# Kernel tuning notes

Hardware: AMD Instinct MI355X
Metric: run time of the kernel (lower is better)

## Reference

```python
import jax, jax.numpy as jnp
import numpy as np

B, H, F, Z, T = 4096, 512, 256, 64, 16
IN = Z + H + F  # LSTM input dim

def _dense_params(key, din, dout, scale=0.05):
    kw, kb = jax.random.split(key)
    return (jax.random.normal(kw, (din, dout), jnp.float32) * scale,
            jax.random.normal(kb, (dout,), jnp.float32) * scale)

def setup_inputs() -> dict:
    key = jax.random.key(0)
    ks = jax.random.split(key, 16)
    inp = {
        'h_i': jax.random.normal(ks[0], (B, H), jnp.float32),
        'eps_inf': jax.random.normal(ks[1], (T, B, Z), jnp.float32),
        'eps_pri': jax.random.normal(ks[2], (T, B, Z), jnp.float32),
        'Wx': jax.random.normal(ks[3], (IN, 4 * H), jnp.float32) * 0.05,
        'Wh': jax.random.normal(ks[4], (H, 4 * H), jnp.float32) * 0.05,
        'b_lstm': jnp.zeros((4 * H,), jnp.float32),
    }
    dims = [(H, F), (F, F), (F, F),            # dense1-3
            (2 * H + 2 * F, Z), (Z, Z), (Z, Z),  # dense4-6 (inference)
            (2 * H + F, Z), (Z, Z), (Z, Z)]      # dense7-9 (prior)
    for i, (di, do) in enumerate(dims):
        w, b = _dense_params(ks[5 + i], di, do)
        inp[f'W{i+1}'] = w
        inp[f'b{i+1}'] = b
    return inp

def reference(h_i, eps_inf, eps_pri, Wx, Wh, b_lstm,
              W1, b1, W2, b2, W3, b3, W4, b4, W5, b5,
              W6, b6, W7, b7, W8, b8, W9, b9):
    relu = jax.nn.relu
    batch = h_i.shape[0]

    def step(carry, eps):
        h, c, z_j, y_prev = carry
        e_inf, e_pri = eps
        x_j = jnp.concatenate([z_j, h_i, y_prev], axis=1)  # [B, Z+H+F]
        gates = x_j @ Wx + h @ Wh + b_lstm                 # [B, 4H]
        i_g, f_g, g_g, o_g = jnp.split(gates, 4, axis=1)   # keras order i,f,c,o
        c_new = jax.nn.sigmoid(f_g) * c + jax.nn.sigmoid(i_g) * jnp.tanh(g_g)
        h_new = jax.nn.sigmoid(o_g) * jnp.tanh(c_new)
        # decoder MLP on LSTM output
        y_j = relu(relu(relu(h_new @ W1 + b1) @ W2 + b2) @ W3 + b3)  # [B, F]
        s_j = c_new  # state[1] is the cell state in keras LSTMCell
        # inference network
        inf_in = jnp.concatenate([h_i, s_j, y_j, y_prev], axis=1)
        h_z = relu(inf_in @ W4 + b4)
        mean_j = relu(h_z @ W5 + b5)
        log_var_j = relu(h_z @ W6 + b6)
        z_new = mean_j + e_inf * jnp.sqrt(jnp.exp(log_var_j))
        # prior network
        pri_in = jnp.concatenate([h_i, s_j, y_prev], axis=1)
        h_z_ = relu(pri_in @ W7 + b7)
        mean_j_ = relu(h_z_ @ W8 + b8)
        log_var_j_ = relu(h_z_ @ W9 + b9)
        z_prior = mean_j_ + e_pri * jnp.sqrt(jnp.exp(log_var_j_))
        return (h_new, c_new, z_new, y_j), (y_j, mean_j, log_var_j, z_new, z_prior)

    init = (jnp.zeros((batch, Wh.shape[0]), h_i.dtype),
            jnp.zeros((batch, Wh.shape[0]), h_i.dtype),
            jnp.zeros((batch, W5.shape[1]), h_i.dtype),
            jnp.zeros((batch, W1.shape[1]), h_i.dtype))
    _, (ys, means, log_vars, z_post, z_pri) = jax.lax.scan(step, init, (eps_inf, eps_pri))
    fake_input = jnp.transpose(ys, (1, 0, 2))     # [B, T, F]
    mean_all = jnp.transpose(means, (1, 0, 2))    # [B, T, Z]
    log_var_all = jnp.transpose(log_vars, (1, 0, 2))
    z_all = jnp.stack([z_post, z_pri], axis=1)    # [T, 2, B, Z]
    return fake_input, mean_all, log_var_all, z_all
```

## Files before the change

kernel.cpp:

```cpp
#include <hip/hip_runtime.h>


typedef __attribute__((ext_vector_type(8))) short short8;
typedef __attribute__((ext_vector_type(4))) float f32x4;

#define Bt 4096
#define Hd 512
#define Fd 256
#define Zd 64
#define Td 16

#define OFF_WG   0
#define OFF_WPH  212992
#define OFF_W1   344064
#define OFF_W2   360448
#define OFF_W3   368640
#define OFF_W4D  376832
#define OFF_W4H  385024
#define OFF_W7D  389120
#define OFF_W7H  395264
#define OFF_W5   399360
#define OFF_W6   399872
#define OFF_W8   400384
#define OFF_W9   400896

#define O1 16777216
#define O2 20971520
#define O3 25165824

__device__ inline short f2bf(float f) {
  unsigned u = __builtin_bit_cast(unsigned, f);
  unsigned r = (u + 0x7FFFu + ((u >> 16) & 1u)) >> 16;
  return (short)(unsigned short)r;
}
__device__ inline float sigm(float x) { return 1.f / (1.f + __expf(-x)); }
__device__ inline float tanhx(float x) { return 1.f - 2.f / (__expf(2.f * x) + 1.f); }

__global__ void conv_frag(const float* s0, int k0, const float* s1, int k1,
                          const float* s2, int k2, int N, short8* dst, int KT,
                          int total) {
  int idx = blockIdx.x * blockDim.x + threadIdx.x;
  if (idx >= total) return;
  int lane = idx & 63;
  int tt = idx >> 6;
  int kt = tt % KT;
  int nt = tt / KT;
  int c = nt * 16 + (lane & 15);
  int kb = kt * 32 + (lane >> 4) * 8;
  short8 v;
#pragma unroll
  for (int j = 0; j < 8; ++j) {
    int kc = kb + j;
    float f;
    if (kc < k0) f = s0[kc * N + c];
    else if (kc < k0 + k1) f = s1[(kc - k0) * N + c];
    else f = s2[(kc - k0 - k1) * N + c];
    v[j] = f2bf(f);
  }
  dst[idx] = v;
}

struct Params {
  const float* h_i; const float* eps_inf; const float* eps_pri;
  const float* b_lstm;
  const float *b1, *b2, *b3, *b4, *b5, *b6, *b7, *b8, *b9;
  const short8 *WG, *WPH, *W1f, *W2f, *W3f, *W4d, *W4h, *W7d, *W7h,
               *W5f, *W6f, *W8f, *W9f;
  float* out;
};

#define A1S 840
#define A4S 1032
#define TS  264
#define HZS 72

#define MFMA(a, b, c) __builtin_amdgcn_mfma_f32_16x16x32_bf16((a), (b), (c), 0, 0, 0)

template <int KT>
__device__ inline f32x4 dense1(const short* Asrc, int astride, int aoff,
                               const short8* W, const float* bias,
                               int nt, int lane) {
  int lrow = lane >> 4, lcol = lane & 15;
  float b = bias[nt * 16 + lcol];
  f32x4 o = (f32x4){b, b, b, b};
  for (int kt = 0; kt < KT; ++kt) {
    short8 a = *(const short8*)&Asrc[lcol * astride + aoff + kt * 32 + lrow * 8];
    short8 w = W[(nt * KT + kt) * 64 + lane];
    o = MFMA(a, w, o);
  }
  return o;
}

__global__ __launch_bounds__(1024, 1) void vrnn_kernel(Params p) {
  __shared__ short A1[16 * A1S];
  __shared__ short A4[16 * A4S];
  __shared__ short T1[16 * TS];
  __shared__ short T2[16 * TS];
  __shared__ short HZi[16 * HZS];
  __shared__ short HZp[16 * HZS];
  __shared__ float Mi[1024], Li[1024], Mp[1024], Lp[1024];

  const int tid = threadIdx.x;
  const int wave = tid >> 6;
  const int lane = tid & 63;
  const int lrow = lane >> 4;
  const int lcol = lane & 15;
  const int rowbase = blockIdx.x * 16;

  f32x4 base[4][2];
  f32x4 cst[2];
  f32x4 base47 = (f32x4){0.f, 0.f, 0.f, 0.f};

  for (int i = tid; i < 16 * 512; i += 1024) {
    int r = i >> 9, c = i & 511;
    A1[r * A1S + 320 + c] = f2bf(p.h_i[(rowbase + r) * Hd + c]);
  }
  for (int i = tid; i < 16 * 320; i += 1024) {
    int r = i / 320, c = i - r * 320;
    A1[r * A1S + c] = 0;
  }
  for (int i = tid; i < 16 * 256; i += 1024) {
    int r = i >> 8, c = i & 255;
    A4[r * A4S + 512 + c] = 0;
  }
  __syncthreads();

#pragma unroll
  for (int g = 0; g < 4; ++g)
#pragma unroll
    for (int j = 0; j < 2; ++j) {
      float b = p.b_lstm[g * 512 + wave * 32 + j * 16 + lcol];
      base[g][j] = (f32x4){b, b, b, b};
    }
  for (int kt = 0; kt < 16; ++kt) {
    short8 a = *(const short8*)&A1[lcol * A1S + 320 + kt * 32 + lrow * 8];
#pragma unroll
    for (int g = 0; g < 4; ++g)
#pragma unroll
      for (int j = 0; j < 2; ++j) {
        int nt = g * 32 + wave * 2 + j;
        short8 w = p.WPH[(nt * 16 + kt) * 64 + lane];
        base[g][j] = MFMA(a, w, base[g][j]);
      }
  }
  if (wave < 8) {
    const short8* W = (wave < 4) ? p.W4h : p.W7h;
    const float* bb = (wave < 4) ? p.b4 : p.b7;
    int nt = wave & 3;
    float b = bb[nt * 16 + lcol];
    base47 = (f32x4){b, b, b, b};
    for (int kt = 0; kt < 16; ++kt) {
      short8 a = *(const short8*)&A1[lcol * A1S + 320 + kt * 32 + lrow * 8];
      short8 w = W[(nt * 16 + kt) * 64 + lane];
      base47 = MFMA(a, w, base47);
    }
  }
  __syncthreads();
  for (int i = tid; i < 16 * 512; i += 1024) {
    int r = i >> 9, c = i & 511;
    A1[r * A1S + 320 + c] = 0;
  }
#pragma unroll
  for (int j = 0; j < 2; ++j) cst[j] = (f32x4){0.f, 0.f, 0.f, 0.f};
  __syncthreads();

  for (int t = 0; t < Td; ++t) {
    f32x4 acc[4][2];
#pragma unroll
    for (int g = 0; g < 4; ++g)
#pragma unroll
      for (int j = 0; j < 2; ++j) acc[g][j] = base[g][j];
#pragma unroll 2
    for (int kt = 0; kt < 26; ++kt) {
      short8 a = *(const short8*)&A1[lcol * A1S + kt * 32 + lrow * 8];
#pragma unroll
      for (int g = 0; g < 4; ++g)
#pragma unroll
        for (int j = 0; j < 2; ++j) {
          int nt = g * 32 + wave * 2 + j;
          short8 w = p.WG[(nt * 26 + kt) * 64 + lane];
          acc[g][j] = MFMA(a, w, acc[g][j]);
        }
    }
    __syncthreads();

#pragma unroll
    for (int j = 0; j < 2; ++j) {
#pragma unroll
      for (int r = 0; r < 4; ++r) {
        float iv = sigm(acc[0][j][r]);
        float fv = sigm(acc[1][j][r]);
        float gv = tanhx(acc[2][j][r]);
        float ov = sigm(acc[3][j][r]);
        float cn = fv * cst[j][r] + iv * gv;
        cst[j][r] = cn;
        float hn = ov * tanhx(cn);
        int row = lrow * 4 + r;
        int col = wave * 32 + j * 16 + lcol;
        A1[row * A1S + 320 + col] = f2bf(hn);
        A4[row * A4S + col] = f2bf(cn);
      }
    }
    __syncthreads();

    {
      f32x4 o = dense1<16>(A1, A1S, 320, p.W1f, p.b1, wave, lane);
#pragma unroll
      for (int r = 0; r < 4; ++r)
        T1[(lrow * 4 + r) * TS + wave * 16 + lcol] = f2bf(fmaxf(o[r], 0.f));
    }
    __syncthreads();
    {
      f32x4 o = dense1<8>(T1, TS, 0, p.W2f, p.b2, wave, lane);
#pragma unroll
      for (int r = 0; r < 4; ++r)
        T2[(lrow * 4 + r) * TS + wave * 16 + lcol] = f2bf(fmaxf(o[r], 0.f));
    }
    __syncthreads();
    {
      f32x4 o = dense1<8>(T2, TS, 0, p.W3f, p.b3, wave, lane);
#pragma unroll
      for (int r = 0; r < 4; ++r) {
        int row = lrow * 4 + r;
        int col = wave * 16 + lcol;
        float v = fmaxf(o[r], 0.f);
        A4[row * A4S + 768 + col] = f2bf(v);
        p.out[(size_t)(rowbase + row) * 4096 + t * 256 + col] = v;
      }
    }
    __syncthreads();

    if (wave < 8) {
      f32x4 hz = base47;
      if (wave < 4) {
        int nt = wave;
        for (int kt = 0; kt < 32; ++kt) {
          short8 a = *(const short8*)&A4[lcol * A4S + kt * 32 + lrow * 8];
          short8 w = p.W4d[(nt * 32 + kt) * 64 + lane];
          hz = MFMA(a, w, hz);
        }
#pragma unroll
        for (int r = 0; r < 4; ++r)
          HZi[(lrow * 4 + r) * HZS + nt * 16 + lcol] = f2bf(fmaxf(hz[r], 0.f));
      } else {
        int nt = wave - 4;
        for (int kt = 0; kt < 24; ++kt) {
          short8 a = *(const short8*)&A4[lcol * A4S + kt * 32 + lrow * 8];
          short8 w = p.W7d[(nt * 24 + kt) * 64 + lane];
          hz = MFMA(a, w, hz);
        }
#pragma unroll
        for (int r = 0; r < 4; ++r)
          HZp[(lrow * 4 + r) * HZS + nt * 16 + lcol] = f2bf(fmaxf(hz[r], 0.f));
      }
    }
    __syncthreads();

    {
      int m = wave >> 2, q = wave & 3;
      const short8* W = (m == 0) ? p.W5f : (m == 1) ? p.W6f : (m == 2) ? p.W8f : p.W9f;
      const float* bb = (m == 0) ? p.b5 : (m == 1) ? p.b6 : (m == 2) ? p.b8 : p.b9;
      const short* As = (m < 2) ? HZi : HZp;
      float b = bb[q * 16 + lcol];
      f32x4 o = (f32x4){b, b, b, b};
#pragma unroll
      for (int kt = 0; kt < 2; ++kt) {
        short8 a = *(const short8*)&As[lcol * HZS + kt * 32 + lrow * 8];
        short8 w = W[(q * 2 + kt) * 64 + lane];
        o = MFMA(a, w, o);
      }
#pragma unroll
      for (int r = 0; r < 4; ++r) {
        int row = lrow * 4 + r;
        int col = q * 16 + lcol;
        float v = fmaxf(o[r], 0.f);
        size_t gb = (size_t)(rowbase + row) * 1024 + t * 64;
        if (m == 0) {
          Mi[row * 64 + col] = v; p.out[O1 + gb + col] = v;
        } else if (m == 1) {
          Li[row * 64 + col] = v; p.out[O2 + gb + col] = v;
        } else if (m == 2) {
          Mp[row * 64 + col] = v;
        } else {
          Lp[row * 64 + col] = v;
        }
      }
    }
    __syncthreads();

    {
      int e = tid;
      int row = e >> 6, col = e & 63;
      int b = rowbase + row;
      float ei = p.eps_inf[((size_t)t * Bt + b) * 64 + col];
      float ep = p.eps_pri[((size_t)t * Bt + b) * 64 + col];
      float zi = Mi[e] + ei * sqrtf(__expf(Li[e]));
      float zp = Mp[e] + ep * sqrtf(__expf(Lp[e]));
      p.out[O3 + ((size_t)(t * 2 + 0) * Bt + b) * 64 + col] = zi;
      p.out[O3 + ((size_t)(t * 2 + 1) * Bt + b) * 64 + col] = zp;
      A1[row * A1S + col] = f2bf(zi);
    }
    for (int i = tid; i < 16 * 256; i += 1024) {
      int r = i >> 8, c = i & 255;
      short v = A4[r * A4S + 768 + c];
      A1[r * A1S + 64 + c] = v;
      A4[r * A4S + 512 + c] = v;
    }
    __syncthreads();
  }
}

extern "C" void kernel_launch(void* const* d_in, const int* in_sizes, int n_in,
                              void* d_out, int out_size, void* d_ws, size_t ws_size,
                              hipStream_t stream) {
  const float* h_i     = (const float*)d_in[0];
  const float* eps_inf = (const float*)d_in[1];
  const float* eps_pri = (const float*)d_in[2];
  const float* Wx      = (const float*)d_in[3];
  const float* Wh      = (const float*)d_in[4];
  const float* b_lstm  = (const float*)d_in[5];
  const float* W1 = (const float*)d_in[6];  const float* b1 = (const float*)d_in[7];
  const float* W2 = (const float*)d_in[8];  const float* b2 = (const float*)d_in[9];
  const float* W3 = (const float*)d_in[10]; const float* b3 = (const float*)d_in[11];
  const float* W4 = (const float*)d_in[12]; const float* b4 = (const float*)d_in[13];
  const float* W5 = (const float*)d_in[14]; const float* b5 = (const float*)d_in[15];
  const float* W6 = (const float*)d_in[16]; const float* b6 = (const float*)d_in[17];
  const float* W7 = (const float*)d_in[18]; const float* b7 = (const float*)d_in[19];
  const float* W8 = (const float*)d_in[20]; const float* b8 = (const float*)d_in[21];
  const float* W9 = (const float*)d_in[22]; const float* b9 = (const float*)d_in[23];
  short8* ws = (short8*)d_ws;
  const float* nil = nullptr;

  auto cv = [&](const float* s0, int k0, const float* s1, int k1,
                const float* s2, int k2, int N, int off, int KT, int NT) {
    int total = NT * KT * 64;
    conv_frag<<<(total + 255) / 256, 256, 0, stream>>>(s0, k0, s1, k1, s2, k2,
                                                       N, ws + off, KT, total);
  };
  cv(Wx, 64, Wx + 576 * 2048, 256, Wh, 512, 2048, OFF_WG, 26, 128);
  cv(Wx + 64 * 2048, 512, nil, 0, nil, 0, 2048, OFF_WPH, 16, 128);
  cv(W1, 512, nil, 0, nil, 0, 256, OFF_W1, 16, 16);
  cv(W2, 256, nil, 0, nil, 0, 256, OFF_W2, 8, 16);
  cv(W3, 256, nil, 0, nil, 0, 256, OFF_W3, 8, 16);
  cv(W4 + 512 * 64, 512, W4 + 1280 * 64, 256, W4 + 1024 * 64, 256, 64, OFF_W4D, 32, 4);
  cv(W4, 512, nil, 0, nil, 0, 64, OFF_W4H, 16, 4);
  cv(W7 + 512 * 64, 512, W7 + 1024 * 64, 256, nil, 0, 64, OFF_W7D, 24, 4);
  cv(W7, 512, nil, 0, nil, 0, 64, OFF_W7H, 16, 4);
  cv(W5, 64, nil, 0, nil, 0, 64, OFF_W5, 2, 4);
  cv(W6, 64, nil, 0, nil, 0, 64, OFF_W6, 2, 4);
  cv(W8, 64, nil, 0, nil, 0, 64, OFF_W8, 2, 4);
  cv(W9, 64, nil, 0, nil, 0, 64, OFF_W9, 2, 4);

  Params P{h_i, eps_inf, eps_pri, b_lstm,
           b1, b2, b3, b4, b5, b6, b7, b8, b9,
           ws + OFF_WG, ws + OFF_WPH, ws + OFF_W1, ws + OFF_W2, ws + OFF_W3,
           ws + OFF_W4D, ws + OFF_W4H, ws + OFF_W7D, ws + OFF_W7H,
           ws + OFF_W5, ws + OFF_W6, ws + OFF_W8, ws + OFF_W9,
           (float*)d_out};
  vrnn_kernel<<<256, 1024, 0, stream>>>(P);
}
```

Measured before the change: 1.835 ms.

## Split LSTM gate columns across paired blocks exchanging state via global flags

Each pair of workgroups now shares 32 batch rows and splits the 4H gate columns in half. Each block streams only half the LSTM weights, reusing every weight fragment across two 16-row MFMA tiles. Partner blocks swap h/c and y/z halves through global scratch with release/acquire flag spin-waits, and the kernel is launched cooperatively so the partners are co-resident. Precomputed h_i gate contributions are kept packed as bf16 to save registers, and the next weight fragments are prefetched one step ahead. In exchange there are two inter-block handshakes per timestep, and the bf16 packing adds rounding.

```diff
diff --git a/kernel.cpp b/kernel.cpp
--- a/kernel.cpp
+++ b/kernel.cpp
@@ -3,15 +3,23 @@
 
 typedef __attribute__((ext_vector_type(8))) short short8;
 typedef __attribute__((ext_vector_type(4))) float f32x4;
+typedef unsigned long long u64;
+typedef __attribute__((ext_vector_type(2))) unsigned long long u64x2;
 
 #define Bt 4096
-#define Hd 512
-#define Fd 256
-#define Zd 64
 #define Td 16
 
-#define OFF_WG   0
-#define OFF_WPH  212992
+#define US 1608
+#define UZ 0
+#define UY 64
+#define UH 320
+#define USs 832
+#define UC 1344
+#define TS 264
+#define HZS 72
+
+#define OFF_WGH  0
+#define OFF_WPHH 212992
 #define OFF_W1   344064
 #define OFF_W2   360448
 #define OFF_W3   368640
@@ -24,6 +32,12 @@
 #define OFF_W8   400384
 #define OFF_W9   400896
 
+#define XH_BYTE  6422528ULL
+#define XC_BYTE  (XH_BYTE + 512ULL*16384)
+#define XY_BYTE  (XC_BYTE + 512ULL*16384)
+#define XZ_BYTE  (XY_BYTE + 512ULL*8192)
+#define FL_BYTE  (XZ_BYTE + 512ULL*2048)
+
 #define O1 16777216
 #define O2 20971520
 #define O3 25165824
@@ -35,276 +49,374 @@
 }
 __device__ inline float sigm(float x) { return 1.f / (1.f + __expf(-x)); }
 __device__ inline float tanhx(float x) { return 1.f - 2.f / (__expf(2.f * x) + 1.f); }
+__device__ inline unsigned pack2(float a, float b) {
+  return (unsigned)(unsigned short)f2bf(a) | ((unsigned)(unsigned short)f2bf(b) << 16);
+}
+__device__ inline f32x4 unpack4(unsigned u0, unsigned u1) {
+  f32x4 r;
+  r[0] = __builtin_bit_cast(float, u0 << 16);
+  r[1] = __builtin_bit_cast(float, u0 & 0xffff0000u);
+  r[2] = __builtin_bit_cast(float, u1 << 16);
+  r[3] = __builtin_bit_cast(float, u1 & 0xffff0000u);
+  return r;
+}
+
+#define MFMA(a, b, c) __builtin_amdgcn_mfma_f32_16x16x32_bf16((a), (b), (c), 0, 0, 0)
 
 __global__ void conv_frag(const float* s0, int k0, const float* s1, int k1,
-                          const float* s2, int k2, int N, short8* dst, int KT,
-                          int total) {
+                          const float* s2, int k2, int N, int col0,
+                          short8* dst, int KT, int total) {
   int idx = blockIdx.x * blockDim.x + threadIdx.x;
   if (idx >= total) return;
   int lane = idx & 63;
   int tt = idx >> 6;
   int kt = tt % KT;
   int nt = tt / KT;
-  int c = nt * 16 + (lane & 15);
+  int c = col0 + nt * 16 + (lane & 15);
   int kb = kt * 32 + (lane >> 4) * 8;
   short8 v;
 #pragma unroll
   for (int j = 0; j < 8; ++j) {
     int kc = kb + j;
     float f;
-    if (kc < k0) f = s0[kc * N + c];
-    else if (kc < k0 + k1) f = s1[(kc - k0) * N + c];
-    else f = s2[(kc - k0 - k1) * N + c];
+    if (kc < k0) f = s0[(size_t)kc * N + c];
+    else if (kc < k0 + k1) f = s1[(size_t)(kc - k0) * N + c];
+    else f = s2[(size_t)(kc - k0 - k1) * N + c];
     v[j] = f2bf(f);
   }
   dst[idx] = v;
 }
+
+__global__ void init_flags(int* f) { if (threadIdx.x < 512) f[threadIdx.x] = 0; }
 
 struct Params {
   const float* h_i; const float* eps_inf; const float* eps_pri;
   const float* b_lstm;
   const float *b1, *b2, *b3, *b4, *b5, *b6, *b7, *b8, *b9;
-  const short8 *WG, *WPH, *W1f, *W2f, *W3f, *W4d, *W4h, *W7d, *W7h,
+  const short8 *WGH, *WPHH, *W1f, *W2f, *W3f, *W4D, *W4H, *W7D, *W7H,
                *W5f, *W6f, *W8f, *W9f;
+  u64 *XH, *XC, *XY, *XZ;
+  int* flags;
   float* out;
 };
 
-#define A1S 840
-#define A4S 1032
-#define TS  264
-#define HZS 72
-
-#define MFMA(a, b, c) __builtin_amdgcn_mfma_f32_16x16x32_bf16((a), (b), (c), 0, 0, 0)
-
-template <int KT>
-__device__ inline f32x4 dense1(const short* Asrc, int astride, int aoff,
-                               const short8* W, const float* bias,
-                               int nt, int lane) {
-  int lrow = lane >> 4, lcol = lane & 15;
-  float b = bias[nt * 16 + lcol];
-  f32x4 o = (f32x4){b, b, b, b};
-  for (int kt = 0; kt < KT; ++kt) {
-    short8 a = *(const short8*)&Asrc[lcol * astride + aoff + kt * 32 + lrow * 8];
-    short8 w = W[(nt * KT + kt) * 64 + lane];
-    o = MFMA(a, w, o);
-  }
-  return o;
-}
-
 __global__ __launch_bounds__(1024, 1) void vrnn_kernel(Params p) {
-  __shared__ short A1[16 * A1S];
-  __shared__ short A4[16 * A4S];
+  __shared__ short U[32 * US];
   __shared__ short T1[16 * TS];
   __shared__ short T2[16 * TS];
-  __shared__ short HZi[16 * HZS];
-  __shared__ short HZp[16 * HZS];
-  __shared__ float Mi[1024], Li[1024], Mp[1024], Lp[1024];
 
   const int tid = threadIdx.x;
-  const int wave = tid >> 6;
+  const int wv = tid >> 6;
   const int lane = tid & 63;
   const int lrow = lane >> 4;
   const int lcol = lane & 15;
-  const int rowbase = blockIdx.x * 16;
-
-  f32x4 base[4][2];
-  f32x4 cst[2];
+  const int bid = blockIdx.x;
+  const int xcd = bid & 7;
+  const int half = xcd >> 2;
+  const int g = (xcd & 3) * 32 + (bid >> 3);
+  const int rowbase = g * 32;
+  const int ownrow0 = half * 16;
+  const int fown = (g * 2 + half) * 2;
+  const int fpar = (g * 2 + (1 - half)) * 2;
+
+  for (int i = tid; i < 32 * 512; i += 1024) {
+    int r = i >> 9, c = i & 511;
+    U[r * US + UH + c] = f2bf(p.h_i[(size_t)(rowbase + r) * 512 + c]);
+  }
+  __syncthreads();
+
+  unsigned base_pk[2][4][2];
+  {
+    const short8* Wb = p.WPHH + (size_t)(half * 4) * 16 * 16 * 64;
+    f32x4 a2[2][4];
+#pragma unroll
+    for (int G = 0; G < 4; ++G) {
+      float b = p.b_lstm[G * 512 + half * 256 + wv * 16 + lcol];
+      a2[0][G] = (f32x4){b, b, b, b};
+      a2[1][G] = (f32x4){b, b, b, b};
+    }
+    for (int kt = 0; kt < 16; ++kt) {
+      short8 a0 = *(const short8*)&U[lcol * US + UH + kt * 32 + lrow * 8];
+      short8 a1 = *(const short8*)&U[(16 + lcol) * US + UH + kt * 32 + lrow * 8];
+#pragma unroll
+      for (int G = 0; G < 4; ++G) {
+        short8 w = Wb[(size_t)((G * 16 + wv) * 16 + kt) * 64 + lane];
+        a2[0][G] = MFMA(a0, w, a2[0][G]);
+        a2[1][G] = MFMA(a1, w, a2[1][G]);
+      }
+    }
+#pragma unroll
+    for (int rh = 0; rh < 2; ++rh)
+#pragma unroll
+      for (int G = 0; G < 4; ++G) {
+        base_pk[rh][G][0] = pack2(a2[rh][G][0], a2[rh][G][1]);
+        base_pk[rh][G][1] = pack2(a2[rh][G][2], a2[rh][G][3]);
+      }
+  }
   f32x4 base47 = (f32x4){0.f, 0.f, 0.f, 0.f};
-
-  for (int i = tid; i < 16 * 512; i += 1024) {
-    int r = i >> 9, c = i & 511;
-    A1[r * A1S + 320 + c] = f2bf(p.h_i[(rowbase + r) * Hd + c]);
-  }
-  for (int i = tid; i < 16 * 320; i += 1024) {
-    int r = i / 320, c = i - r * 320;
-    A1[r * A1S + c] = 0;
-  }
-  for (int i = tid; i < 16 * 256; i += 1024) {
-    int r = i >> 8, c = i & 255;
-    A4[r * A4S + 512 + c] = 0;
-  }
-  __syncthreads();
-
-#pragma unroll
-  for (int g = 0; g < 4; ++g)
-#pragma unroll
-    for (int j = 0; j < 2; ++j) {
-      float b = p.b_lstm[g * 512 + wave * 32 + j * 16 + lcol];
-      base[g][j] = (f32x4){b, b, b, b};
-    }
-  for (int kt = 0; kt < 16; ++kt) {
-    short8 a = *(const short8*)&A1[lcol * A1S + 320 + kt * 32 + lrow * 8];
-#pragma unroll
-    for (int g = 0; g < 4; ++g)
-#pragma unroll
-      for (int j = 0; j < 2; ++j) {
-        int nt = g * 32 + wave * 2 + j;
-        short8 w = p.WPH[(nt * 16 + kt) * 64 + lane];
-        base[g][j] = MFMA(a, w, base[g][j]);
-      }
-  }
-  if (wave < 8) {
-    const short8* W = (wave < 4) ? p.W4h : p.W7h;
-    const float* bb = (wave < 4) ? p.b4 : p.b7;
-    int nt = wave & 3;
-    float b = bb[nt * 16 + lcol];
+  if (wv < 8) {
+    int net = wv >> 2, q = wv & 3;
+    const short8* W = net ? p.W7H : p.W4H;
+    const float* bb = net ? p.b7 : p.b4;
+    float b = bb[q * 16 + lcol];
     base47 = (f32x4){b, b, b, b};
     for (int kt = 0; kt < 16; ++kt) {
-      short8 a = *(const short8*)&A1[lcol * A1S + 320 + kt * 32 + lrow * 8];
-      short8 w = W[(nt * 16 + kt) * 64 + lane];
+      short8 a = *(const short8*)&U[(ownrow0 + lcol) * US + UH + kt * 32 + lrow * 8];
+      short8 w = W[(q * 16 + kt) * 64 + lane];
       base47 = MFMA(a, w, base47);
     }
   }
   __syncthreads();
-  for (int i = tid; i < 16 * 512; i += 1024) {
-    int r = i >> 9, c = i & 511;
-    A1[r * A1S + 320 + c] = 0;
-  }
-#pragma unroll
-  for (int j = 0; j < 2; ++j) cst[j] = (f32x4){0.f, 0.f, 0.f, 0.f};
+  for (int i = tid; i < 6400; i += 1024) {
+    int r = i / 200, c8 = i % 200;
+    *(short8*)&U[r * US + c8 * 8] = (short8){0, 0, 0, 0, 0, 0, 0, 0};
+  }
+  f32x4 cst[2];
+  cst[0] = (f32x4){0.f, 0.f, 0.f, 0.f};
+  cst[1] = (f32x4){0.f, 0.f, 0.f, 0.f};
   __syncthreads();
 
   for (int t = 0; t < Td; ++t) {
-    f32x4 acc[4][2];
-#pragma unroll
-    for (int g = 0; g < 4; ++g)
-#pragma unroll
-      for (int j = 0; j < 2; ++j) acc[g][j] = base[g][j];
-#pragma unroll 2
-    for (int kt = 0; kt < 26; ++kt) {
-      short8 a = *(const short8*)&A1[lcol * A1S + kt * 32 + lrow * 8];
-#pragma unroll
-      for (int g = 0; g < 4; ++g)
-#pragma unroll
-        for (int j = 0; j < 2; ++j) {
-          int nt = g * 32 + wave * 2 + j;
-          short8 w = p.WG[(nt * 26 + kt) * 64 + lane];
-          acc[g][j] = MFMA(a, w, acc[g][j]);
-        }
-    }
-    __syncthreads();
-
-#pragma unroll
-    for (int j = 0; j < 2; ++j) {
+    const int par = t & 1;
+    f32x4 acc[2][4];
+#pragma unroll
+    for (int rh = 0; rh < 2; ++rh)
+#pragma unroll
+      for (int G = 0; G < 4; ++G)
+        acc[rh][G] = unpack4(base_pk[rh][G][0], base_pk[rh][G][1]);
+    {
+      const short8* Wg = p.WGH + (size_t)(half * 4) * 16 * 26 * 64;
+      short8 w[4], wn[4];
+#pragma unroll
+      for (int G = 0; G < 4; ++G)
+        w[G] = Wg[(size_t)((G * 16 + wv) * 26) * 64 + lane];
+      for (int kt = 0; kt < 26; ++kt) {
+        short8 a0 = *(const short8*)&U[lcol * US + kt * 32 + lrow * 8];
+        short8 a1 = *(const short8*)&U[(16 + lcol) * US + kt * 32 + lrow * 8];
+        if (kt < 25) {
+#pragma unroll
+          for (int G = 0; G < 4; ++G)
+            wn[G] = Wg[(size_t)((G * 16 + wv) * 26 + kt + 1) * 64 + lane];
+        }
+#pragma unroll
+        for (int G = 0; G < 4; ++G) {
+          acc[0][G] = MFMA(a0, w[G], acc[0][G]);
+          acc[1][G] = MFMA(a1, w[G], acc[1][G]);
+        }
+#pragma unroll
+        for (int G = 0; G < 4; ++G) w[G] = wn[G];
+      }
+    }
+    __syncthreads();
+
+    {
+      int hc = half * 256 + wv * 16 + lcol;
+#pragma unroll
+      for (int rh = 0; rh < 2; ++rh)
+#pragma unroll
+        for (int r = 0; r < 4; ++r) {
+          float iv = sigm(acc[rh][0][r]);
+          float fv = sigm(acc[rh][1][r]);
+          float gv = tanhx(acc[rh][2][r]);
+          float ov = sigm(acc[rh][3][r]);
+          float cn = fv * cst[rh][r] + iv * gv;
+          cst[rh][r] = cn;
+          float hn = ov * tanhx(cn);
+          int row = rh * 16 + lrow * 4 + r;
+          U[row * US + UH + hc] = f2bf(hn);
+          U[row * US + USs + hc] = f2bf(cn);
+        }
+    }
+    __syncthreads();
+    {
+      u64* xh = p.XH + (size_t)((g * 2 + half) * 2 + par) * 2048;
+      u64* xc = p.XC + (size_t)((g * 2 + half) * 2 + par) * 2048;
+      int row = tid >> 5, c8 = tid & 31;
+      short8 hv = *(const short8*)&U[row * US + UH + half * 256 + c8 * 8];
+      short8 cv = *(const short8*)&U[row * US + USs + half * 256 + c8 * 8];
+      u64x2 h2 = __builtin_bit_cast(u64x2, hv);
+      u64x2 c2 = __builtin_bit_cast(u64x2, cv);
+      __hip_atomic_store(&xh[tid * 2 + 0], h2[0], __ATOMIC_RELAXED, __HIP_MEMORY_SCOPE_AGENT);
+      __hip_atomic_store(&xh[tid * 2 + 1], h2[1], __ATOMIC_RELAXED, __HIP_MEMORY_SCOPE_AGENT);
+      __hip_atomic_store(&xc[tid * 2 + 0], c2[0], __ATOMIC_RELAXED, __HIP_MEMORY_SCOPE_AGENT);
+      __hip_atomic_store(&xc[tid * 2 + 1], c2[1], __ATOMIC_RELAXED, __HIP_MEMORY_SCOPE_AGENT);
+    }
+    __syncthreads();
+    if (tid == 0) {
+      __hip_atomic_fetch_add(&p.flags[fown + 0], 1, __ATOMIC_RELEASE, __HIP_MEMORY_SCOPE_AGENT);
+      while (__hip_atomic_load(&p.flags[fpar + 0], __ATOMIC_ACQUIRE, __HIP_MEMORY_SCOPE_AGENT) < t + 1)
+        __builtin_amdgcn_s_sleep(1);
+    }
+    __syncthreads();
+    {
+      u64* xh = p.XH + (size_t)((g * 2 + (1 - half)) * 2 + par) * 2048;
+      u64* xc = p.XC + (size_t)((g * 2 + (1 - half)) * 2 + par) * 2048;
+      int row = tid >> 5, c8 = tid & 31;
+      u64x2 h2, c2;
+      h2[0] = __hip_atomic_load(&xh[tid * 2 + 0], __ATOMIC_RELAXED, __HIP_MEMORY_SCOPE_AGENT);
+      h2[1] = __hip_atomic_load(&xh[tid * 2 + 1], __ATOMIC_RELAXED, __HIP_MEMORY_SCOPE_AGENT);
+      c2[0] = __hip_atomic_load(&xc[tid * 2 + 0], __ATOMIC_RELAXED, __HIP_MEMORY_SCOPE_AGENT);
+      c2[1] = __hip_atomic_load(&xc[tid * 2 + 1], __ATOMIC_RELAXED, __HIP_MEMORY_SCOPE_AGENT);
+      *(short8*)&U[row * US + UH + (1 - half) * 256 + c8 * 8] = __builtin_bit_cast(short8, h2);
+      *(short8*)&U[row * US + USs + (1 - half) * 256 + c8 * 8] = __builtin_bit_cast(short8, c2);
+    }
+    __syncthreads();
+
+    {
+      float b = p.b1[wv * 16 + lcol];
+      f32x4 o = (f32x4){b, b, b, b};
+      for (int kt = 0; kt < 16; ++kt) {
+        short8 a = *(const short8*)&U[(ownrow0 + lcol) * US + UH + kt * 32 + lrow * 8];
+        o = MFMA(a, p.W1f[(wv * 16 + kt) * 64 + lane], o);
+      }
+#pragma unroll
+      for (int r = 0; r < 4; ++r)
+        T1[(lrow * 4 + r) * TS + wv * 16 + lcol] = f2bf(fmaxf(o[r], 0.f));
+    }
+    __syncthreads();
+    {
+      float b = p.b2[wv * 16 + lcol];
+      f32x4 o = (f32x4){b, b, b, b};
+      for (int kt = 0; kt < 8; ++kt) {
+        short8 a = *(const short8*)&T1[lcol * TS + kt * 32 + lrow * 8];
+        o = MFMA(a, p.W2f[(wv * 8 + kt) * 64 + lane], o);
+      }
+#pragma unroll
+      for (int r = 0; r < 4; ++r)
+        T2[(lrow * 4 + r) * TS + wv * 16 + lcol] = f2bf(fmaxf(o[r], 0.f));
+    }
+    __syncthreads();
+    {
+      float b = p.b3[wv * 16 + lcol];
+      f32x4 o = (f32x4){b, b, b, b};
+      for (int kt = 0; kt < 8; ++kt) {
+        short8 a = *(const short8*)&T2[lcol * TS + kt * 32 + lrow * 8];
+        o = MFMA(a, p.W3f[(wv * 8 + kt) * 64 + lane], o);
+      }
 #pragma unroll
       for (int r = 0; r < 4; ++r) {
-        float iv = sigm(acc[0][j][r]);
-        float fv = sigm(acc[1][j][r]);
-        float gv = tanhx(acc[2][j][r]);
-        float ov = sigm(acc[3][j][r]);
-        float cn = fv * cst[j][r] + iv * gv;
-        cst[j][r] = cn;
-        float hn = ov * tanhx(cn);
-        int row = lrow * 4 + r;
-        int col = wave * 32 + j * 16 + lcol;
-        A1[row * A1S + 320 + col] = f2bf(hn);
-        A4[row * A4S + col] = f2bf(cn);
-      }
-    }
-    __syncthreads();
-
-    {
-      f32x4 o = dense1<16>(A1, A1S, 320, p.W1f, p.b1, wave, lane);
-#pragma unroll
-      for (int r = 0; r < 4; ++r)
-        T1[(lrow * 4 + r) * TS + wave * 16 + lcol] = f2bf(fmaxf(o[r], 0.f));
-    }
-    __syncthreads();
-    {
-      f32x4 o = dense1<8>(T1, TS, 0, p.W2f, p.b2, wave, lane);
-#pragma unroll
-      for (int r = 0; r < 4; ++r)
-        T2[(lrow * 4 + r) * TS + wave * 16 + lcol] = f2bf(fmaxf(o[r], 0.f));
-    }
-    __syncthreads();
-    {
-      f32x4 o = dense1<8>(T2, TS, 0, p.W3f, p.b3, wave, lane);
+        int crow = lrow * 4 + r;
+        float v = fmaxf(o[r], 0.f);
+        U[(ownrow0 + crow) * US + UC + wv * 16 + lcol] = f2bf(v);
+        p.out[(size_t)(rowbase + ownrow0 + crow) * 4096 + t * 256 + wv * 16 + lcol] = v;
+      }
+    }
+    __syncthreads();
+
+    if (wv < 8) {
+      int net = wv >> 2, q = wv & 3;
+      f32x4 hz = base47;
+      if (net == 0) {
+        for (int kt = 0; kt < 32; ++kt) {
+          int kk = kt < 16 ? USs + 32 * kt : (kt < 24 ? UC + 32 * (kt - 16) : UY + 32 * (kt - 24));
+          short8 a = *(const short8*)&U[(ownrow0 + lcol) * US + kk + lrow * 8];
+          hz = MFMA(a, p.W4D[(q * 32 + kt) * 64 + lane], hz);
+        }
+#pragma unroll
+        for (int r = 0; r < 4; ++r)
+          T1[(lrow * 4 + r) * HZS + q * 16 + lcol] = f2bf(fmaxf(hz[r], 0.f));
+      } else {
+        for (int kt = 0; kt < 24; ++kt) {
+          int kk = kt < 16 ? USs + 32 * kt : UY + 32 * (kt - 16);
+          short8 a = *(const short8*)&U[(ownrow0 + lcol) * US + kk + lrow * 8];
+          hz = MFMA(a, p.W7D[(q * 24 + kt) * 64 + lane], hz);
+        }
+#pragma unroll
+        for (int r = 0; r < 4; ++r)
+          T2[(lrow * 4 + r) * HZS + q * 16 + lcol] = f2bf(fmaxf(hz[r], 0.f));
+      }
+    }
+    __syncthreads();
+
+    if (wv < 8) {
+      int net = wv >> 2, q = wv & 3;
+      const short8* Wm = net ? p.W8f : p.W5f;
+      const short8* Wl = net ? p.W9f : p.W6f;
+      const float* bm = net ? p.b8 : p.b5;
+      const float* bl = net ? p.b9 : p.b6;
+      const short* HZ = net ? T2 : T1;
+      float b0 = bm[q * 16 + lcol], b1v = bl[q * 16 + lcol];
+      f32x4 om = (f32x4){b0, b0, b0, b0};
+      f32x4 ol = (f32x4){b1v, b1v, b1v, b1v};
+#pragma unroll
+      for (int kt = 0; kt < 2; ++kt) {
+        short8 a = *(const short8*)&HZ[lcol * HZS + kt * 32 + lrow * 8];
+        om = MFMA(a, Wm[(q * 2 + kt) * 64 + lane], om);
+        ol = MFMA(a, Wl[(q * 2 + kt) * 64 + lane], ol);
+      }
+      const float* eps = net ? p.eps_pri : p.eps_inf;
 #pragma unroll
       for (int r = 0; r < 4; ++r) {
-        int row = lrow * 4 + r;
-        int col = wave * 16 + lcol;
-        float v = fmaxf(o[r], 0.f);
-        A4[row * A4S + 768 + col] = f2bf(v);
-        p.out[(size_t)(rowbase + row) * 4096 + t * 256 + col] = v;
-      }
-    }
-    __syncthreads();
-
-    if (wave < 8) {
-      f32x4 hz = base47;
-      if (wave < 4) {
-        int nt = wave;
-        for (int kt = 0; kt < 32; ++kt) {
-          short8 a = *(const short8*)&A4[lcol * A4S + kt * 32 + lrow * 8];
-          short8 w = p.W4d[(nt * 32 + kt) * 64 + lane];
-          hz = MFMA(a, w, hz);
-        }
-#pragma unroll
-        for (int r = 0; r < 4; ++r)
-          HZi[(lrow * 4 + r) * HZS + nt * 16 + lcol] = f2bf(fmaxf(hz[r], 0.f));
+        int crow = lrow * 4 + r;
+        int grow = rowbase + ownrow0 + crow;
+        int col = q * 16 + lcol;
+        float mv = fmaxf(om[r], 0.f), lv = fmaxf(ol[r], 0.f);
+        float ev = eps[((size_t)t * Bt + grow) * 64 + col];
+        float zv = mv + ev * sqrtf(__expf(lv));
+        if (net == 0) {
+          size_t gb = (size_t)grow * 1024 + t * 64 + col;
+          p.out[O1 + gb] = mv;
+          p.out[O2 + gb] = lv;
+          p.out[O3 + ((size_t)(t * 2 + 0) * Bt + grow) * 64 + col] = zv;
+          U[(ownrow0 + crow) * US + UZ + col] = f2bf(zv);
+        } else {
+          p.out[O3 + ((size_t)(t * 2 + 1) * Bt + grow) * 64 + col] = zv;
+        }
+      }
+    }
+    __syncthreads();
+    {
+      int slot = (g * 2 + half) * 2 + par;
+      if (tid >= 512) {
+        int i = tid - 512;
+        int row = i >> 5, c8 = i & 31;
+        short8 v = *(const short8*)&U[(ownrow0 + row) * US + UC + c8 * 8];
+        u64x2 v2 = __builtin_bit_cast(u64x2, v);
+        u64* xy = p.XY + (size_t)slot * 1024;
+        __hip_atomic_store(&xy[i * 2 + 0], v2[0], __ATOMIC_RELAXED, __HIP_MEMORY_SCOPE_AGENT);
+        __hip_atomic_store(&xy[i * 2 + 1], v2[1], __ATOMIC_RELAXED, __HIP_MEMORY_SCOPE_AGENT);
+      } else if (tid < 128) {
+        int row = tid >> 3, c8 = tid & 7;
+        short8 v = *(const short8*)&U[(ownrow0 + row) * US + UZ + c8 * 8];
+        u64x2 v2 = __builtin_bit_cast(u64x2, v);
+        u64* xz = p.XZ + (size_t)slot * 256;
+        __hip_atomic_store(&xz[tid * 2 + 0], v2[0], __ATOMIC_RELAXED, __HIP_MEMORY_SCOPE_AGENT);
+        __hip_atomic_store(&xz[tid * 2 + 1], v2[1], __ATOMIC_RELAXED, __HIP_MEMORY_SCOPE_AGENT);
+      }
+    }
+    __syncthreads();
+    if (tid == 0) {
+      __hip_atomic_fetch_add(&p.flags[fown + 1], 1, __ATOMIC_RELEASE, __HIP_MEMORY_SCOPE_AGENT);
+      while (__hip_atomic_load(&p.flags[fpar + 1], __ATOMIC_ACQUIRE, __HIP_MEMORY_SCOPE_AGENT) < t + 1)
+        __builtin_amdgcn_s_sleep(1);
+    }
+    __syncthreads();
+    {
+      int pslot = (g * 2 + (1 - half)) * 2 + par;
+      int prow0 = (1 - half) * 16;
+      u64* xy = p.XY + (size_t)pslot * 1024;
+      u64* xz = p.XZ + (size_t)pslot * 256;
+      if (tid < 512) {
+        int row = tid >> 5, c8 = tid & 31;
+        u64x2 v2;
+        v2[0] = __hip_atomic_load(&xy[tid * 2 + 0], __ATOMIC_RELAXED, __HIP_MEMORY_SCOPE_AGENT);
+        v2[1] = __hip_atomic_load(&xy[tid * 2 + 1], __ATOMIC_RELAXED, __HIP_MEMORY_SCOPE_AGENT);
+        *(short8*)&U[(prow0 + row) * US + UY + c8 * 8] = __builtin_bit_cast(short8, v2);
+      } else if (tid < 640) {
+        int i = tid - 512;
+        int row = i >> 3, c8 = i & 7;
+        u64x2 v2;
+        v2[0] = __hip_atomic_load(&xz[i * 2 + 0], __ATOMIC_RELAXED, __HIP_MEMORY_SCOPE_AGENT);
+        v2[1] = __hip_atomic_load(&xz[i * 2 + 1], __ATOMIC_RELAXED, __HIP_MEMORY_SCOPE_AGENT);
+        *(short8*)&U[(prow0 + row) * US + UZ + c8 * 8] = __builtin_bit_cast(short8, v2);
       } else {
-        int nt = wave - 4;
-        for (int kt = 0; kt < 24; ++kt) {
-          short8 a = *(const short8*)&A4[lcol * A4S + kt * 32 + lrow * 8];
-          short8 w = p.W7d[(nt * 24 + kt) * 64 + lane];
-          hz = MFMA(a, w, hz);
-        }
-#pragma unroll
-        for (int r = 0; r < 4; ++r)
-          HZp[(lrow * 4 + r) * HZS + nt * 16 + lcol] = f2bf(fmaxf(hz[r], 0.f));
-      }
-    }
-    __syncthreads();
-
-    {
-      int m = wave >> 2, q = wave & 3;
-      const short8* W = (m == 0) ? p.W5f : (m == 1) ? p.W6f : (m == 2) ? p.W8f : p.W9f;
-      const float* bb = (m == 0) ? p.b5 : (m == 1) ? p.b6 : (m == 2) ? p.b8 : p.b9;
-      const short* As = (m < 2) ? HZi : HZp;
-      float b = bb[q * 16 + lcol];
-      f32x4 o = (f32x4){b, b, b, b};
-#pragma unroll
-      for (int kt = 0; kt < 2; ++kt) {
-        short8 a = *(const short8*)&As[lcol * HZS + kt * 32 + lrow * 8];
-        short8 w = W[(q * 2 + kt) * 64 + lane];
-        o = MFMA(a, w, o);
-      }
-#pragma unroll
-      for (int r = 0; r < 4; ++r) {
-        int row = lrow * 4 + r;
-        int col = q * 16 + lcol;
-        float v = fmaxf(o[r], 0.f);
-        size_t gb = (size_t)(rowbase + row) * 1024 + t * 64;
-        if (m == 0) {
-          Mi[row * 64 + col] = v; p.out[O1 + gb + col] = v;
-        } else if (m == 1) {
-          Li[row * 64 + col] = v; p.out[O2 + gb + col] = v;
-        } else if (m == 2) {
-          Mp[row * 64 + col] = v;
-        } else {
-          Lp[row * 64 + col] = v;
-        }
-      }
-    }
-    __syncthreads();
-
-    {
-      int e = tid;
-      int row = e >> 6, col = e & 63;
-      int b = rowbase + row;
-      float ei = p.eps_inf[((size_t)t * Bt + b) * 64 + col];
-      float ep = p.eps_pri[((size_t)t * Bt + b) * 64 + col];
-      float zi = Mi[e] + ei * sqrtf(__expf(Li[e]));
-      float zp = Mp[e] + ep * sqrtf(__expf(Lp[e]));
-      p.out[O3 + ((size_t)(t * 2 + 0) * Bt + b) * 64 + col] = zi;
-      p.out[O3 + ((size_t)(t * 2 + 1) * Bt + b) * 64 + col] = zp;
-      A1[row * A1S + col] = f2bf(zi);
-    }
-    for (int i = tid; i < 16 * 256; i += 1024) {
-      int r = i >> 8, c = i & 255;
-      short v = A4[r * A4S + 768 + c];
-      A1[r * A1S + 64 + c] = v;
-      A4[r * A4S + 512 + c] = v;
+        int i = tid - 640;
+        for (; i < 512; i += 384) {
+          int row = i >> 5, c8 = i & 31;
+          short8 v = *(const short8*)&U[(ownrow0 + row) * US + UC + c8 * 8];
+          *(short8*)&U[(ownrow0 + row) * US + UY + c8 * 8] = v;
+        }
+      }
     }
     __syncthreads();
   }
@@ -329,33 +441,47 @@
   const float* W8 = (const float*)d_in[20]; const float* b8 = (const float*)d_in[21];
   const float* W9 = (const float*)d_in[22]; const float* b9 = (const float*)d_in[23];
   short8* ws = (short8*)d_ws;
+  char* wsb = (char*)d_ws;
   const float* nil = nullptr;
 
   auto cv = [&](const float* s0, int k0, const float* s1, int k1,
-                const float* s2, int k2, int N, int off, int KT, int NT) {
+                const float* s2, int k2, int N, int col0, int off, int KT, int NT) {
     int total = NT * KT * 64;
     conv_frag<<<(total + 255) / 256, 256, 0, stream>>>(s0, k0, s1, k1, s2, k2,
-                                                       N, ws + off, KT, total);
+                                                       N, col0, ws + off, KT, total);
   };
-  cv(Wx, 64, Wx + 576 * 2048, 256, Wh, 512, 2048, OFF_WG, 26, 128);
-  cv(Wx + 64 * 2048, 512, nil, 0, nil, 0, 2048, OFF_WPH, 16, 128);
-  cv(W1, 512, nil, 0, nil, 0, 256, OFF_W1, 16, 16);
-  cv(W2, 256, nil, 0, nil, 0, 256, OFF_W2, 8, 16);
-  cv(W3, 256, nil, 0, nil, 0, 256, OFF_W3, 8, 16);
-  cv(W4 + 512 * 64, 512, W4 + 1280 * 64, 256, W4 + 1024 * 64, 256, 64, OFF_W4D, 32, 4);
-  cv(W4, 512, nil, 0, nil, 0, 64, OFF_W4H, 16, 4);
-  cv(W7 + 512 * 64, 512, W7 + 1024 * 64, 256, nil, 0, 64, OFF_W7D, 24, 4);
-  cv(W7, 512, nil, 0, nil, 0, 64, OFF_W7H, 16, 4);
-  cv(W5, 64, nil, 0, nil, 0, 64, OFF_W5, 2, 4);
-  cv(W6, 64, nil, 0, nil, 0, 64, OFF_W6, 2, 4);
-  cv(W8, 64, nil, 0, nil, 0, 64, OFF_W8, 2, 4);
-  cv(W9, 64, nil, 0, nil, 0, 64, OFF_W9, 2, 4);
-
-  Params P{h_i, eps_inf, eps_pri, b_lstm,
-           b1, b2, b3, b4, b5, b6, b7, b8, b9,
-           ws + OFF_WG, ws + OFF_WPH, ws + OFF_W1, ws + OFF_W2, ws + OFF_W3,
-           ws + OFF_W4D, ws + OFF_W4H, ws + OFF_W7D, ws + OFF_W7H,
-           ws + OFF_W5, ws + OFF_W6, ws + OFF_W8, ws + OFF_W9,
-           (float*)d_out};
-  vrnn_kernel<<<256, 1024, 0, stream>>>(P);
-}
+  for (int half = 0; half < 2; ++half)
+    for (int G = 0; G < 4; ++G) {
+      int col0 = G * 512 + half * 256;
+      cv(Wx, 64, Wx + 576 * 2048, 256, Wh, 512, 2048, col0,
+         OFF_WGH + (half * 4 + G) * 16 * 26 * 64, 26, 16);
+      cv(Wx + 64 * 2048, 512, nil, 0, nil, 0, 2048, col0,
+         OFF_WPHH + (half * 4 + G) * 16 * 16 * 64, 16, 16);
+    }
+  cv(W1, 512, nil, 0, nil, 0, 256, 0, OFF_W1, 16, 16);
+  cv(W2, 256, nil, 0, nil, 0, 256, 0, OFF_W2, 8, 16);
+  cv(W3, 256, nil, 0, nil, 0, 256, 0, OFF_W3, 8, 16);
+  cv(W4 + 512 * 64, 512, W4 + 1024 * 64, 256, W4 + 1280 * 64, 256, 64, 0, OFF_W4D, 32, 4);
+  cv(W4, 512, nil, 0, nil, 0, 64, 0, OFF_W4H, 16, 4);
+  cv(W7 + 512 * 64, 512, W7 + 1024 * 64, 256, nil, 0, 64, 0, OFF_W7D, 24, 4);
+  cv(W7, 512, nil, 0, nil, 0, 64, 0, OFF_W7H, 16, 4);
+  cv(W5, 64, nil, 0, nil, 0, 64, 0, OFF_W5, 2, 4);
+  cv(W6, 64, nil, 0, nil, 0, 64, 0, OFF_W6, 2, 4);
+  cv(W8, 64, nil, 0, nil, 0, 64, 0, OFF_W8, 2, 4);
+  cv(W9, 64, nil, 0, nil, 0, 64, 0, OFF_W9, 2, 4);
+
+  int* flags = (int*)(wsb + FL_BYTE);
+  init_flags<<<1, 512, 0, stream>>>(flags);
+
+  static Params P;
+  P = Params{h_i, eps_inf, eps_pri, b_lstm,
+             b1, b2, b3, b4, b5, b6, b7, b8, b9,
+             ws + OFF_WGH, ws + OFF_WPHH, ws + OFF_W1, ws + OFF_W2, ws + OFF_W3,
+             ws + OFF_W4D, ws + OFF_W4H, ws + OFF_W7D, ws + OFF_W7H,
+             ws + OFF_W5, ws + OFF_W6, ws + OFF_W8, ws + OFF_W9,
+             (u64*)(wsb + XH_BYTE), (u64*)(wsb + XC_BYTE),
+             (u64*)(wsb + XY_BYTE), (u64*)(wsb + XZ_BYTE),
+             flags, (float*)d_out};
+  void* args[] = {&P};
+  hipLaunchCooperativeKernel((void*)vrnn_kernel, dim3(256), dim3(1024), args, 0, stream);
+}
```

Result: slower. 2.872 ms (+56.5%).

## Double-buffer LSTM gate weights, stagger k-start per block, pack base in bf16

Applied to the files above, without the earlier changes.

The LSTM gate GEMM loop is rewritten as a two-stage register double buffer: weight fragments for the next k-tiles are loaded from global memory while MFMAs run on the current ones. Each group of blocks starts at a different k offset (rotated by block index) so concurrent blocks spread their requests over different parts of the weight matrix instead of all reading the same tile at once. The precomputed h_i/bias gate contribution is now stored packed as bf16 in registers, which frees VGPRs but rounds that term. The launch bound is raised from 1 to 4 blocks, asking the compiler to cut register use.

```diff
diff --git a/kernel.cpp b/kernel.cpp
--- a/kernel.cpp
+++ b/kernel.cpp
@@ -35,6 +35,17 @@
 }
 __device__ inline float sigm(float x) { return 1.f / (1.f + __expf(-x)); }
 __device__ inline float tanhx(float x) { return 1.f - 2.f / (__expf(2.f * x) + 1.f); }
+__device__ inline unsigned pack2(float a, float b) {
+  return (unsigned)(unsigned short)f2bf(a) | ((unsigned)(unsigned short)f2bf(b) << 16);
+}
+__device__ inline f32x4 unpack4(unsigned u0, unsigned u1) {
+  f32x4 r;
+  r[0] = __builtin_bit_cast(float, u0 << 16);
+  r[1] = __builtin_bit_cast(float, u0 & 0xffff0000u);
+  r[2] = __builtin_bit_cast(float, u1 << 16);
+  r[3] = __builtin_bit_cast(float, u1 & 0xffff0000u);
+  return r;
+}
 
 __global__ void conv_frag(const float* s0, int k0, const float* s1, int k1,
                           const float* s2, int k2, int N, short8* dst, int KT,
@@ -91,7 +102,7 @@
   return o;
 }
 
-__global__ __launch_bounds__(1024, 1) void vrnn_kernel(Params p) {
+__global__ __launch_bounds__(1024, 4) void vrnn_kernel(Params p) {
   __shared__ short A1[16 * A1S];
   __shared__ short A4[16 * A4S];
   __shared__ short T1[16 * TS];
@@ -106,8 +117,10 @@
   const int lrow = lane >> 4;
   const int lcol = lane & 15;
   const int rowbase = blockIdx.x * 16;
-
-  f32x4 base[4][2];
+  const int xrank = (blockIdx.x >> 3) & 31;
+  const int ktA0 = (xrank * 26) >> 5;
+
+  unsigned base_pk[4][2][2];
   f32x4 cst[2];
   f32x4 base47 = (f32x4){0.f, 0.f, 0.f, 0.f};
 
@@ -125,22 +138,32 @@
   }
   __syncthreads();
 
-#pragma unroll
-  for (int g = 0; g < 4; ++g)
-#pragma unroll
-    for (int j = 0; j < 2; ++j) {
-      float b = p.b_lstm[g * 512 + wave * 32 + j * 16 + lcol];
-      base[g][j] = (f32x4){b, b, b, b};
-    }
-  for (int kt = 0; kt < 16; ++kt) {
-    short8 a = *(const short8*)&A1[lcol * A1S + 320 + kt * 32 + lrow * 8];
+  {
+    f32x4 bse[4][2];
 #pragma unroll
     for (int g = 0; g < 4; ++g)
 #pragma unroll
       for (int j = 0; j < 2; ++j) {
-        int nt = g * 32 + wave * 2 + j;
-        short8 w = p.WPH[(nt * 16 + kt) * 64 + lane];
-        base[g][j] = MFMA(a, w, base[g][j]);
+        float b = p.b_lstm[g * 512 + wave * 32 + j * 16 + lcol];
+        bse[g][j] = (f32x4){b, b, b, b};
+      }
+    for (int kt = 0; kt < 16; ++kt) {
+      short8 a = *(const short8*)&A1[lcol * A1S + 320 + kt * 32 + lrow * 8];
+#pragma unroll
+      for (int g = 0; g < 4; ++g)
+#pragma unroll
+        for (int j = 0; j < 2; ++j) {
+          int nt = g * 32 + wave * 2 + j;
+          short8 w = p.WPH[(nt * 16 + kt) * 64 + lane];
+          bse[g][j] = MFMA(a, w, bse[g][j]);
+        }
+    }
+#pragma unroll
+    for (int g = 0; g < 4; ++g)
+#pragma unroll
+      for (int j = 0; j < 2; ++j) {
+        base_pk[g][j][0] = pack2(bse[g][j][0], bse[g][j][1]);
+        base_pk[g][j][1] = pack2(bse[g][j][2], bse[g][j][3]);
       }
   }
   if (wave < 8) {
@@ -169,18 +192,58 @@
 #pragma unroll
     for (int g = 0; g < 4; ++g)
 #pragma unroll
-      for (int j = 0; j < 2; ++j) acc[g][j] = base[g][j];
-#pragma unroll 2
-    for (int kt = 0; kt < 26; ++kt) {
-      short8 a = *(const short8*)&A1[lcol * A1S + kt * 32 + lrow * 8];
-#pragma unroll
-      for (int g = 0; g < 4; ++g)
-#pragma unroll
-        for (int j = 0; j < 2; ++j) {
-          int nt = g * 32 + wave * 2 + j;
-          short8 w = p.WG[(nt * 26 + kt) * 64 + lane];
-          acc[g][j] = MFMA(a, w, acc[g][j]);
-        }
+      for (int j = 0; j < 2; ++j)
+        acc[g][j] = unpack4(base_pk[g][j][0], base_pk[g][j][1]);
+    {
+      short8 wA[8], wB[8];
+      int ka = ktA0;
+      int kb = ka + 1; if (kb >= 26) kb -= 26;
+#pragma unroll
+      for (int G = 0; G < 4; ++G)
+#pragma unroll
+        for (int j = 0; j < 2; ++j)
+          wA[G * 2 + j] =
+              p.WG[(size_t)((G * 32 + wave * 2 + j) * 26 + ka) * 64 + lane];
+#pragma unroll
+      for (int G = 0; G < 4; ++G)
+#pragma unroll
+        for (int j = 0; j < 2; ++j)
+          wB[G * 2 + j] =
+              p.WG[(size_t)((G * 32 + wave * 2 + j) * 26 + kb) * 64 + lane];
+      for (int kt = 0; kt < 26; kt += 2) {
+        int kc = kb + 1; if (kc >= 26) kc -= 26;
+        int kd = kc + 1; if (kd >= 26) kd -= 26;
+        short8 a = *(const short8*)&A1[lcol * A1S + ka * 32 + lrow * 8];
+#pragma unroll
+        for (int G = 0; G < 4; ++G)
+#pragma unroll
+          for (int j = 0; j < 2; ++j)
+            acc[G][j] = MFMA(a, wA[G * 2 + j], acc[G][j]);
+        if (kt + 2 < 26) {
+#pragma unroll
+          for (int G = 0; G < 4; ++G)
+#pragma unroll
+            for (int j = 0; j < 2; ++j)
+              wA[G * 2 + j] =
+                  p.WG[(size_t)((G * 32 + wave * 2 + j) * 26 + kc) * 64 + lane];
+        }
+        short8 a2 = *(const short8*)&A1[lcol * A1S + kb * 32 + lrow * 8];
+#pragma unroll
+        for (int G = 0; G < 4; ++G)
+#pragma unroll
+          for (int j = 0; j < 2; ++j)
+            acc[G][j] = MFMA(a2, wB[G * 2 + j], acc[G][j]);
+        if (kt + 3 < 26) {
+#pragma unroll
+          for (int G = 0; G < 4; ++G)
+#pragma unroll
+            for (int j = 0; j < 2; ++j)
+              wB[G * 2 + j] =
+                  p.WG[(size_t)((G * 32 + wave * 2 + j) * 26 + kd) * 64 + lane];
+        }
+        ka = kc;
+        kb = kd;
+      }
     }
     __syncthreads();
 
```

Result: slower. 3.296 ms (+79.6%).
